# Kernel tuning notes

Hardware: AMD Instinct MI355X
Metric: run time of the kernel (lower is better)

## Reference

```python
import jax, jax.numpy as jnp
import numpy as np

B, C, N, T = 8, 32, 4000, 12
KT = 3
TS = 6          # tem_size
SUP_ORD_CH = (2 * 3 + 1) * C  # (order*support_len+1)*c_in = 224
EPS = 1e-5


def setup_inputs() -> dict:
    key = jax.random.key(0)
    ks = jax.random.split(key, 20)
    inp = {
        "x": jax.random.normal(ks[0], (B, C, N, T), dtype=jnp.float32),
        # dense normalized supports (scaled uniform, like row-normalized adjacency)
        "A0": jax.random.uniform(ks[1], (N, N), dtype=jnp.float32) / N,
        "A1": jax.random.uniform(ks[2], (N, N), dtype=jnp.float32) / N,
        "A2": jax.random.uniform(ks[3], (N, N), dtype=jnp.float32) / N,
        # conv1: 1x1 Conv2d(32 -> 32), bias
        "conv1_w": jax.random.normal(ks[4], (C, C), dtype=jnp.float32) * 0.05,
        "conv1_b": jnp.zeros((C,), dtype=jnp.float32),
        # multigcn mlp: Conv2d(224 -> 64, kernel (1, Kt)), bias
        "mlp_w": jax.random.normal(ks[5], (2 * C, SUP_ORD_CH, 1, KT), dtype=jnp.float32) * 0.02,
        "mlp_b": jnp.zeros((2 * C,), dtype=jnp.float32),
        # conv_temp1: 1x1 Conv2d over time axis (10 -> 6), bias
        "ct1_w": jax.random.normal(ks[6], (TS, T - KT + 1), dtype=jnp.float32) * 0.1,
        "ct1_b": jnp.zeros((TS,), dtype=jnp.float32),
        # TATT_1 params
        "tat_c1_w": jax.random.normal(ks[7], (C,), dtype=jnp.float32) * 0.1,   # Conv2d(c_in->1,1x1,no bias)
        "tat_c2_w": jax.random.normal(ks[8], (N,), dtype=jnp.float32) * 0.01,  # Conv2d(N->1,1x1,no bias)
        "tat_w": jax.random.normal(ks[9], (N, C), dtype=jnp.float32) * 0.01,
        "tat_bias": jnp.zeros((TS, TS), dtype=jnp.float32),
        "tat_v": jax.random.normal(ks[10], (TS, TS), dtype=jnp.float32) * 0.3,
        "bn1_g": jnp.ones((TS,), dtype=jnp.float32),
        "bn1_b": jnp.zeros((TS,), dtype=jnp.float32),
        # final BatchNorm2d(c_out)
        "bn2_g": jnp.ones((C,), dtype=jnp.float32),
        "bn2_b": jnp.zeros((C,), dtype=jnp.float32),
    }
    return inp


def reference(x, A0, A1, A2, conv1_w, conv1_b, mlp_w, mlp_b, ct1_w, ct1_b,
              tat_c1_w, tat_c2_w, tat_w, tat_bias, tat_v, bn1_g, bn1_b,
              bn2_g, bn2_b):
    # residual = conv1(x)  (1x1 conv over channels)
    residual = jnp.einsum('oc,bcnl->bonl', conv1_w, x) + conv1_b[None, :, None, None]

    # multi_gcn_time: nconv does A<-A.T then einsum('ncvl,vw->ncwl'),
    # i.e. out[..,w,..] = sum_v x[..,v,..] * A[w,v]
    outs = [x]
    for A in (A0, A1, A2):
        x1 = jnp.einsum('bcvl,wv->bcwl', x, A)
        outs.append(x1)
        x2 = jnp.einsum('bcvl,wv->bcwl', x1, A)
        outs.append(x2)
    h = jnp.concatenate(outs, axis=1)  # (B, 224, N, T)
    h = jax.lax.conv_general_dilated(
        h, mlp_w, window_strides=(1, 1), padding='VALID',
        dimension_numbers=('NCHW', 'OIHW', 'NCHW')) + mlp_b[None, :, None, None]  # (B,64,N,10)

    # gated tanh * sigmoid
    x1, x2 = jnp.split(h, 2, axis=1)
    g = jnp.tanh(x1) * jax.nn.sigmoid(x2)  # (B,32,N,10)

    # conv_temp1: 1x1 conv over the TIME axis (10 -> 6)
    g = jnp.einsum('ql,bcnl->bcnq', ct1_w, g) + ct1_b[None, None, None, :]  # (B,32,N,6)

    # TATT_1 temporal attention coefficients
    f1 = jnp.einsum('c,bcnt->btn', tat_c1_w, g)                       # (B,6,N)
    f2 = jnp.einsum('n,bcnt->bct', tat_c2_w, g)                       # (B,32,6)
    logits = jax.nn.sigmoid(jnp.einsum('btn,nc,bcs->bts', f1, tat_w, f2) + tat_bias)
    logits = jnp.einsum('ts,bsq->btq', tat_v, logits)                 # (B,6,6)
    # BatchNorm1d(tem_size) applied after permute(0,2,1): channel = q axis
    lp = jnp.transpose(logits, (0, 2, 1))
    mu = lp.mean(axis=(0, 2), keepdims=True)
    var = lp.var(axis=(0, 2), keepdims=True)
    lp = (lp - mu) / jnp.sqrt(var + EPS) * bn1_g[None, :, None] + bn1_b[None, :, None]
    logits = jnp.transpose(lp, (0, 2, 1))
    coefs = jax.nn.softmax(logits, axis=-1)                           # (B,6,6)

    # x = einsum('bcnl,blq->bcnq', x, T_coef.transpose(-1,-2))
    Tc = jnp.transpose(coefs, (0, 2, 1))
    out = jnp.einsum('bcnl,blq->bcnq', g, Tc)                         # (B,32,N,6)

    y = out + residual[:, :, :, -out.shape[3]:]
    # BatchNorm2d(c_out), training-mode batch stats
    mu2 = y.mean(axis=(0, 2, 3), keepdims=True)
    var2 = y.var(axis=(0, 2, 3), keepdims=True)
    return (y - mu2) / jnp.sqrt(var2 + EPS) * bn2_g[None, :, None, None] + bn2_b[None, :, None, None]
```

## Files before the change

### kernel.cpp

```cpp
#include <hip/hip_runtime.h>
#include <hip/hip_bf16.h>
#include <cstdint>
#include <cstddef>


typedef __attribute__((ext_vector_type(8))) short s16x8;
typedef __attribute__((ext_vector_type(4))) short s16x4;
typedef __attribute__((ext_vector_type(4))) float f32x4;

#define DEVFN __device__ __forceinline__

DEVFN void gload16(const void* g, void* l) {
  __builtin_amdgcn_global_load_lds((const __attribute__((address_space(1))) unsigned int*)g,
                                   (__attribute__((address_space(3))) unsigned int*)l, 16, 0, 0);
}

DEVFN unsigned short f2bf(float f) {
  union { float f; unsigned int u; } v; v.f = f;
  unsigned int u = v.u;
  return (unsigned short)((u + 0x7fffu + ((u >> 16) & 1u)) >> 16);
}

__global__ void k_transpose(const float* __restrict__ x,
                            unsigned short* __restrict__ Xt,
                            unsigned short* __restrict__ Scat) {
  __shared__ float ldsT[32 * 417];
  int v0 = blockIdx.x * 32;
  int b = blockIdx.y;
  int tid = threadIdx.x;
  for (int i = tid; i < 1024; i += 256) {
    int c = i >> 5, vv = i & 31;
    const float* src = x + ((size_t)(b * 32 + c) * 4000 + v0 + vv) * 12;
    f32x4 a0 = *(const f32x4*)(src);
    f32x4 a1 = *(const f32x4*)(src + 4);
    f32x4 a2 = *(const f32x4*)(src + 8);
    float* d = ldsT + c * 417 + vv * 13;
    d[0] = a0.x; d[1] = a0.y; d[2] = a0.z; d[3] = a0.w;
    d[4] = a1.x; d[5] = a1.y; d[6] = a1.z; d[7] = a1.w;
    d[8] = a2.x; d[9] = a2.y; d[10] = a2.z; d[11] = a2.w;
  }
  __syncthreads();
  for (int unit = tid; unit < 384; unit += 256) {
    int l = unit >> 5, c = unit & 31;
    alignas(16) unsigned short tmp[32];
#pragma unroll
    for (int vv = 0; vv < 32; ++vv) tmp[vv] = f2bf(ldsT[c * 417 + vv * 13 + l]);
    unsigned short* dst = Xt + (size_t)(b * 384 + l * 32 + c) * 4096 + v0;
#pragma unroll
    for (int j = 0; j < 4; ++j) *(s16x8*)(dst + j * 8) = *(const s16x8*)(tmp + j * 8);
  }
  for (int unit = tid; unit < 384; unit += 256) {
    int l = unit >> 5, vv = unit & 31;
    alignas(16) unsigned short tmp[32];
#pragma unroll
    for (int c = 0; c < 32; ++c) tmp[c] = f2bf(ldsT[c * 417 + vv * 13 + l]);
    unsigned short* dst = Scat + ((size_t)(b * 4000 + v0 + vv) * 12 + l) * 224;
#pragma unroll
    for (int j = 0; j < 4; ++j) *(s16x8*)(dst + j * 8) = *(const s16x8*)(tmp + j * 8);
  }
}

__global__ void k_castA(const float* __restrict__ A, unsigned short* __restrict__ Abf) {
  int idx = blockIdx.x * 256 + threadIdx.x;
  int r = idx >> 10;
  int c4 = (idx & 1023) << 2;
  alignas(8) unsigned short o[4] = {0, 0, 0, 0};
  if (r < 4000 && c4 < 4000) {
    f32x4 v = *(const f32x4*)(A + (size_t)r * 4000 + c4);
    o[0] = f2bf(v.x); o[1] = f2bf(v.y); o[2] = f2bf(v.z); o[3] = f2bf(v.w);
  }
  *(s16x4*)(Abf + (size_t)r * 4096 + c4) = *(const s16x4*)o;
}

__global__ void k_wcat(const float* __restrict__ mlp_w, unsigned short* __restrict__ Wcat) {
  int i = blockIdx.x * 256 + threadIdx.x;
  if (i >= 64 * 672) return;
  int oc = i / 672, k = i % 672;
  int kt = k / 224, ic = k % 224;
  Wcat[i] = f2bf(mlp_w[((size_t)oc * 224 + ic) * 3 + kt]);
}

#define MFMA_(a, b, c) __builtin_amdgcn_mfma_f32_16x16x32_bf16(a, b, c, 0, 0, 0)

#define STGA(d, t) do {                                                          \
    const unsigned short* _s = aSrc + (size_t)(t) * 64;                          \
    unsigned short* _l = smem + (d) * 12288;                                     \
    gload16(_s,          _l + tid * 8);                                          \
    gload16(_s + 262144, _l + (512 + tid) * 8);                                  \
    gload16(_s + 524288, _l + (1024 + tid) * 8);                                 \
  } while (0)

#define STGB(d, h, t) do {                                                       \
    const unsigned short* _s = bSrc + (size_t)(h) * 524288 + (size_t)(t) * 64;   \
    unsigned short* _l = smem + 24576 + ((d) * 2 + (h)) * 8192;                  \
    gload16(_s,          _l + tid * 8);                                          \
    gload16(_s + 262144, _l + (512 + tid) * 8);                                  \
  } while (0)

#define LDA_(d, f, kk) (*(const s16x8*)(smem + (d) * 12288 + aoff + (f) * 1024 + ((kk) ? sxor : 0)))
#define LDB_(d, nf, kk) (*(const s16x8*)(smem + 24576 + ((d) * 2 + hb) * 8192 + boff + (nf) * 1024 + ((kk) ? sxor : 0)))

#define PHASE(d, mp, FIRST, STAGE_CODE, VM) do {                                 \
    s16x8 a00 = LDA_(d, 2 * (mp), 0),     a01 = LDA_(d, 2 * (mp), 1);            \
    s16x8 a10 = LDA_(d, 2 * (mp) + 1, 0), a11 = LDA_(d, 2 * (mp) + 1, 1);        \
    if (FIRST) {                                                                 \
      _Pragma("unroll")                                                          \
      for (int nf = 0; nf < 4; ++nf) { bfr[nf][0] = LDB_(d, nf, 0); bfr[nf][1] = LDB_(d, nf, 1); } \
    }                                                                            \
    STAGE_CODE;                                                                  \
    if (VM) asm volatile("s_waitcnt vmcnt(2)" ::: "memory");                     \
    __builtin_amdgcn_s_barrier();                                                \
    asm volatile("s_waitcnt lgkmcnt(0)" ::: "memory");                           \
    __builtin_amdgcn_s_setprio(1);                                               \
    _Pragma("unroll")                                                            \
    for (int nf = 0; nf < 4; ++nf) {                                             \
      acc[2 * (mp)][nf]     = MFMA_(a00, bfr[nf][0], acc[2 * (mp)][nf]);         \
      acc[2 * (mp)][nf]     = MFMA_(a01, bfr[nf][1], acc[2 * (mp)][nf]);         \
      acc[2 * (mp) + 1][nf] = MFMA_(a10, bfr[nf][0], acc[2 * (mp) + 1][nf]);     \
      acc[2 * (mp) + 1][nf] = MFMA_(a11, bfr[nf][1], acc[2 * (mp) + 1][nf]);     \
    }                                                                            \
    __builtin_amdgcn_s_setprio(0);                                               \
  } while (0)

template <int WRITE_C1>
__global__ __launch_bounds__(512, 2)
void k_gemm(const unsigned short* __restrict__ P, const unsigned short* __restrict__ Q,
            unsigned short* __restrict__ C1, unsigned short* __restrict__ Scat, int jcol) {
  extern __shared__ unsigned short smem[];
  int tid = threadIdx.x;
  int w = tid >> 6, lane = tid & 63;
  int lr = lane & 15, g = lane >> 4;
  int mq = w >> 2, nq = w & 3;
  int bid = blockIdx.x;
  int xcd = bid & 7, lid = bid >> 3;
  int nt = xcd * 2 + (lid >> 4);
  int mt = lid & 15;
  int m0 = mt * 192, n0 = nt * 256;
  int hb = nq >> 1;
  int slot0 = (g ^ (lr & 7)) * 8;
  int sxor = (slot0 & 32) ? -32 : 32;
  int aoff = (mq * 96 + lr) * 64 + slot0;
  int boff = ((nq & 1) * 64 + lr) * 64 + slot0;
  int gk = ((tid & 7) ^ ((tid >> 3) & 7)) * 8;
  const unsigned short* aSrc = P + (size_t)(m0 + (tid >> 3)) * 4096 + gk;
  const unsigned short* bSrc = Q + (size_t)(n0 + (tid >> 3)) * 4096 + gk;
  f32x4 acc[6][4] = {};
  s16x8 bfr[4][2];

  STGA(0, 0);
  STGB(0, 0, 0); STGB(0, 1, 0);
  STGB(1, 0, 1);
  asm volatile("s_waitcnt vmcnt(2)" ::: "memory");
  __builtin_amdgcn_s_barrier();

#pragma unroll 1
  for (int i = 0; i < 32; ++i) {
    int t1 = 2 * i + 1, t2 = 2 * i + 2, t3 = 2 * i + 3;
    PHASE(0, 0, 1, STGB(1, 1, t1), 0);
    PHASE(0, 1, 0, STGA(1, t1),    0);
    PHASE(0, 2, 0, STGB(0, 0, t2), 1);
    PHASE(1, 0, 1, STGB(0, 1, t2), 0);
    PHASE(1, 1, 0, STGA(0, t2),    0);
    PHASE(1, 2, 0, STGB(1, 0, t3), 1);
  }

  asm volatile("s_waitcnt vmcnt(0) lgkmcnt(0)" ::: "memory");
  __syncthreads();
  unsigned short* eld = smem;
  int rb = g * 4;
#pragma unroll
  for (int f = 0; f < 6; ++f)
#pragma unroll
    for (int nf = 0; nf < 4; ++nf)
#pragma unroll
      for (int r = 0; r < 4; ++r)
        eld[(mq * 96 + f * 16 + rb + r) * 264 + nq * 64 + nf * 16 + lr] = f2bf(acc[f][nf][r]);
  __syncthreads();
  if (WRITE_C1) {
#pragma unroll
    for (int uu = 0; uu < 2; ++uu) {
      int u = uu * 512 + tid;
      if (u < 768) {
        int row = u >> 2, q = u & 3;
        unsigned short* dst = C1 + (size_t)(m0 + row) * 4096 + n0 + q * 64;
        const unsigned short* sp = eld + row * 264 + q * 64;
#pragma unroll
        for (int j = 0; j < 8; ++j) *(s16x8*)(dst + j * 8) = *(const s16x8*)(sp + j * 8);
      }
    }
  }
  int bb2 = m0 / 384, lb = (m0 % 384) >> 5;
#pragma unroll
  for (int uu = 0; uu < 3; ++uu) {
    int u = uu * 512 + tid;
    int lg = u >> 8, nl = u & 255;
    int node = n0 + nl;
    if (node < 4000) {
      alignas(16) unsigned short tmp[32];
#pragma unroll
      for (int c = 0; c < 32; ++c) tmp[c] = eld[(lg * 32 + c) * 264 + nl];
      unsigned short* d2 = Scat + ((size_t)(bb2 * 4000 + node) * 12 + lb + lg) * 224 + jcol;
#pragma unroll
      for (int j = 0; j < 4; ++j) *(s16x8*)(d2 + j * 8) = *(const s16x8*)(tmp + j * 8);
    }
  }
}

#define MLPSTG(L, BUF) do {                                                   \
    _Pragma("unroll")                                                         \
    for (int j = 0; j < 7; ++j) {                                             \
      int u = j * 256 + tid;                                                  \
      int s = u >> 6, bn = u & 63;                                            \
      gload16(Scat + ((size_t)(bn0 + bn) * 12 + (L)) * 224 + s * 8,           \
              lds + (BUF) * 14336 + u * 8);                                   \
    }                                                                         \
  } while (0)

__global__ __launch_bounds__(256, 2)
void k_mlp(const unsigned short* __restrict__ Wcat, const unsigned short* __restrict__ Scat,
           const float* __restrict__ mlp_b, float* __restrict__ G) {
  __shared__ unsigned short lds[2 * 14336];
  int tid = threadIdx.x;
  int bn0 = blockIdx.x * 64;
  int w = tid >> 6, lane = tid & 63;
  int lr = lane & 15, g = lane >> 4;
  int p = w & 1, q = w >> 1;
  const unsigned short* w1 = Wcat + (size_t)(p * 16 + lr) * 672 + g * 8;
  const unsigned short* w2 = w1 + 32 * 672;
  f32x4 acc[3][4];

  MLPSTG(0, 0);
  asm volatile("s_waitcnt vmcnt(0)" ::: "memory");
  __syncthreads();

#pragma unroll
  for (int l = 0; l < 12; ++l) {
    if (l < 11) MLPSTG(l + 1, (l + 1) & 1);
    if (l <= 9) {
#pragma unroll
      for (int f = 0; f < 4; ++f) acc[l % 3][f] = (f32x4){0.f, 0.f, 0.f, 0.f};
    }
    const unsigned short* sb = lds + (l & 1) * 14336;
#pragma unroll
    for (int kt = 0; kt < 3; ++kt) {
      int t = l - kt;
      if (t < 0 || t > 9) continue;
      int st = t % 3;
#pragma unroll
      for (int ks = 0; ks < 7; ++ks) {
        s16x8 a1 = *(const s16x8*)(w1 + kt * 224 + ks * 32);
        s16x8 a2 = *(const s16x8*)(w2 + kt * 224 + ks * 32);
        const unsigned short* bbase = sb + ((ks * 4 + g) * 64 + q * 32 + lr) * 8;
        s16x8 b0 = *(const s16x8*)(bbase);
        s16x8 b1 = *(const s16x8*)(bbase + 128);
        acc[st][0] = MFMA_(a1, b0, acc[st][0]);
        acc[st][1] = MFMA_(a1, b1, acc[st][1]);
        acc[st][2] = MFMA_(a2, b0, acc[st][2]);
        acc[st][3] = MFMA_(a2, b1, acc[st][3]);
      }
    }
    if (l >= 2) {
      int t = l - 2, st = t % 3;
#pragma unroll
      for (int bf = 0; bf < 2; ++bf) {
        int nglob = bn0 + q * 32 + bf * 16 + lr;
        int b = nglob / 4000, nn = nglob - b * 4000;
        float* gout = G + ((size_t)(b * 10 + t) * 32) * 4096 + nn;
#pragma unroll
        for (int r = 0; r < 4; ++r) {
          int c = p * 16 + g * 4 + r;
          float v1 = acc[st][bf][r] + mlp_b[c];
          float v2 = acc[st][2 + bf][r] + mlp_b[c + 32];
          gout[(size_t)c * 4096] = tanhf(v1) * (1.0f / (1.0f + __expf(-v2)));
        }
      }
    }
    asm volatile("s_waitcnt vmcnt(0)" ::: "memory");
    __syncthreads();
  }
}

__global__ void k_ct1(const float* __restrict__ G, const float* __restrict__ ct1_w,
                      const float* __restrict__ ct1_b, float* __restrict__ g6) {
  int idx = blockIdx.x * 256 + threadIdx.x;
  if (idx >= 8 * 32 * 4000) return;
  int n = idx % 4000;
  int c = (idx / 4000) % 32;
  int b = idx / (4000 * 32);
  const float* gp = G + ((size_t)(b * 10) * 32 + c) * 4096 + n;
  float v[10];
#pragma unroll
  for (int l = 0; l < 10; ++l) v[l] = gp[(size_t)l * 32 * 4096];
  float* o = g6 + (size_t)idx * 6;
#pragma unroll
  for (int q = 0; q < 6; ++q) {
    float a = ct1_b[q];
#pragma unroll
    for (int l = 0; l < 10; ++l) a += ct1_w[q * 10 + l] * v[l];
    o[q] = a;
  }
}

__global__ void k_f1(const float* __restrict__ g6, const float* __restrict__ c1,
                     float* __restrict__ f1) {
  int idx = blockIdx.x * 128 + threadIdx.x;
  if (idx >= 8 * 4000) return;
  int n = idx % 4000, b = idx / 4000;
  float acc[6] = {};
  const float* gp = g6 + ((size_t)b * 32 * 4000 + n) * 6;
  for (int c = 0; c < 32; ++c) {
    float wv = c1[c];
    const float* p = gp + (size_t)c * 4000 * 6;
#pragma unroll
    for (int t = 0; t < 6; ++t) acc[t] += wv * p[t];
  }
  for (int t = 0; t < 6; ++t) f1[((size_t)b * 6 + t) * 4000 + n] = acc[t];
}

__global__ void k_f2(const float* __restrict__ g6, const float* __restrict__ c2,
                     float* __restrict__ f2) {
  __shared__ float red[256 * 6];
  int bc = blockIdx.x;
  int tid = threadIdx.x;
  float acc[6] = {};
  const float* gp = g6 + (size_t)bc * 4000 * 6;
  for (int n = tid; n < 4000; n += 256) {
    float wv = c2[n];
#pragma unroll
    for (int t = 0; t < 6; ++t) acc[t] += wv * gp[(size_t)n * 6 + t];
  }
  for (int t = 0; t < 6; ++t) red[tid * 6 + t] = acc[t];
  __syncthreads();
  for (int s = 128; s > 0; s >>= 1) {
    if (tid < s)
      for (int t = 0; t < 6; ++t) red[tid * 6 + t] += red[(tid + s) * 6 + t];
    __syncthreads();
  }
  if (tid < 6) f2[bc * 6 + tid] = red[tid];
}

__global__ void k_m1(const float* __restrict__ f1, const float* __restrict__ tw,
                     float* __restrict__ m1) {
  __shared__ float red[8][32];
  int bt = blockIdx.x;
  int nc = blockIdx.y;
  int tid = threadIdx.x;
  int c = tid & 31, gi = tid >> 5;
  float acc = 0.f;
  const float* fp = f1 + (size_t)bt * 4000 + nc * 250;
  const float* twp = tw + ((size_t)nc * 250) * 32 + c;
  for (int n = gi; n < 250; n += 8) acc += fp[n] * twp[n * 32];
  red[gi][c] = acc;
  __syncthreads();
  if (tid < 32) {
    float s = 0.f;
#pragma unroll
    for (int gg = 0; gg < 8; ++gg) s += red[gg][c];
    atomicAdd(&m1[(size_t)bt * 32 + c], s);
  }
}

__global__ void k_att(const float* __restrict__ m1, const float* __restrict__ f2,
                      const float* __restrict__ bias, const float* __restrict__ tv,
                      const float* __restrict__ g1, const float* __restrict__ b1,
                      float* __restrict__ coefs) {
  __shared__ float sig[48 * 6], lgs[48 * 6], mu[6], iv[6];
  int tid = threadIdx.x;
  int b = tid / 6, t = tid % 6;
  if (tid < 48) {
    for (int s = 0; s < 6; ++s) {
      float a = bias[t * 6 + s];
      for (int c = 0; c < 32; ++c)
        a += m1[((size_t)b * 6 + t) * 32 + c] * f2[((size_t)b * 32 + c) * 6 + s];
      sig[tid * 6 + s] = 1.0f / (1.0f + __expf(-a));
    }
  }
  __syncthreads();
  if (tid < 48) {
    for (int q = 0; q < 6; ++q) {
      float a = 0.f;
      for (int s = 0; s < 6; ++s) a += tv[t * 6 + s] * sig[(b * 6 + s) * 6 + q];
      lgs[tid * 6 + q] = a;
    }
  }
  __syncthreads();
  if (tid < 6) {
    float s = 0, s2 = 0;
    for (int r = 0; r < 48; ++r) { float v = lgs[r * 6 + tid]; s += v; s2 += v * v; }
    float m = s / 48.f;
    mu[tid] = m;
    iv[tid] = rsqrtf(s2 / 48.f - m * m + 1e-5f);
  }
  __syncthreads();
  if (tid < 48) {
    float v[6], mx = -1e30f;
    for (int q = 0; q < 6; ++q) {
      v[q] = (lgs[tid * 6 + q] - mu[q]) * iv[q] * g1[q] + b1[q];
      mx = fmaxf(mx, v[q]);
    }
    float s = 0;
    for (int q = 0; q < 6; ++q) { v[q] = __expf(v[q] - mx); s += v[q]; }
    float inv = 1.0f / s;
    for (int q = 0; q < 6; ++q) coefs[tid * 6 + q] = v[q] * inv;
  }
}

__global__ void k_final1(const float* __restrict__ x, const float* __restrict__ cw,
                         const float* __restrict__ cb, const float* __restrict__ g6,
                         const float* __restrict__ coefs, float* __restrict__ out) {
  __shared__ float xt[32 * 8 * 6];
  __shared__ float cwT[1024];
  __shared__ float cfs[36], cbs[32];
  int n0 = blockIdx.x * 8;
  int b = blockIdx.y;
  int tid = threadIdx.x;
  {
    int ci = tid >> 3, seg = tid & 7;
    const float* xp = x + ((size_t)(b * 32 + ci) * 4000 + n0 + seg) * 12 + 6;
#pragma unroll
    for (int q = 0; q < 6; ++q) xt[(ci * 8 + seg) * 6 + q] = xp[q];
  }
  for (int i = tid; i < 1024; i += 256) { int o = i >> 5, ci = i & 31; cwT[ci * 32 + o] = cw[i]; }
  if (tid < 36) cfs[tid] = coefs[b * 36 + tid];
  if (tid < 32) cbs[tid] = cb[tid];
  __syncthreads();
  int nn = tid & 7, c = tid >> 3;
  const float* gp = g6 + ((size_t)(b * 32 + c) * 4000 + n0 + nn) * 6;
  float gv[6];
#pragma unroll
  for (int l = 0; l < 6; ++l) gv[l] = gp[l];
  float y[6];
#pragma unroll
  for (int q = 0; q < 6; ++q) {
    float at = 0.f;
#pragma unroll
    for (int l = 0; l < 6; ++l) at += gv[l] * cfs[q * 6 + l];
    y[q] = at + cbs[c];
  }
  for (int ci = 0; ci < 32; ++ci) {
    float wv = cwT[ci * 32 + c];
#pragma unroll
    for (int q = 0; q < 6; ++q) y[q] += wv * xt[(ci * 8 + nn) * 6 + q];
  }
  float* op = out + ((size_t)(b * 32 + c) * 4000 + n0 + nn) * 6;
#pragma unroll
  for (int q = 0; q < 6; ++q) op[q] = y[q];
}

__global__ void k_stats(const float* __restrict__ out, float* __restrict__ stats) {
  __shared__ float r1[4], r2[4];
  int bc = blockIdx.y;
  int c = bc & 31;
  int tid = threadIdx.x;
  const float* p = out + (size_t)bc * 24000 + blockIdx.x * 6000;
  float s = 0.f, s2 = 0.f;
  for (int i = tid * 4; i < 6000; i += 1024) {
    f32x4 v = *(const f32x4*)(p + i);
    s  += v.x + v.y + v.z + v.w;
    s2 += v.x * v.x + v.y * v.y + v.z * v.z + v.w * v.w;
  }
#pragma unroll
  for (int off = 32; off > 0; off >>= 1) {
    s  += __shfl_down(s, off);
    s2 += __shfl_down(s2, off);
  }
  int lane = tid & 63, w = tid >> 6;
  if (lane == 0) { r1[w] = s; r2[w] = s2; }
  __syncthreads();
  if (tid == 0) {
    atomicAdd(&stats[c],      r1[0] + r1[1] + r1[2] + r1[3]);
    atomicAdd(&stats[32 + c], r2[0] + r2[1] + r2[2] + r2[3]);
  }
}

__global__ void k_final2(float* __restrict__ out, const float* __restrict__ stats,
                         const float* __restrict__ g2, const float* __restrict__ b2) {
  int idx = (blockIdx.x * 256 + threadIdx.x) * 4;
  if (idx >= 6144000) return;
  int c = (idx / 24000) % 32;
  float mean = stats[c] * (1.0f / 192000.f);
  float var = stats[32 + c] * (1.0f / 192000.f) - mean * mean;
  float sc = rsqrtf(var + 1e-5f) * g2[c];
  float sh = b2[c] - mean * sc;
  f32x4 v = *(f32x4*)(out + idx);
  v.x = v.x * sc + sh; v.y = v.y * sc + sh; v.z = v.z * sc + sh; v.w = v.w * sc + sh;
  *(f32x4*)(out + idx) = v;
}

extern "C" void kernel_launch(void* const* d_in, const int* in_sizes, int n_in,
                              void* d_out, int out_size, void* d_ws, size_t ws_size,
                              hipStream_t stream) {
  (void)in_sizes; (void)n_in; (void)out_size;
  const float* x       = (const float*)d_in[0];
  const float* A[3]    = {(const float*)d_in[1], (const float*)d_in[2], (const float*)d_in[3]};
  const float* conv1_w = (const float*)d_in[4];
  const float* conv1_b = (const float*)d_in[5];
  const float* mlp_w   = (const float*)d_in[6];
  const float* mlp_b   = (const float*)d_in[7];
  const float* ct1_w   = (const float*)d_in[8];
  const float* ct1_b   = (const float*)d_in[9];
  const float* c1w     = (const float*)d_in[10];
  const float* c2w     = (const float*)d_in[11];
  const float* tw      = (const float*)d_in[12];
  const float* tbias   = (const float*)d_in[13];
  const float* tv      = (const float*)d_in[14];
  const float* bn1g    = (const float*)d_in[15];
  const float* bn1b    = (const float*)d_in[16];
  const float* bn2g    = (const float*)d_in[17];
  const float* bn2b    = (const float*)d_in[18];
  float* out = (float*)d_out;

  char* ws = (char*)d_ws;
  size_t off = 0;
  auto alloc = [&](size_t bytes) { size_t r = off; off += (bytes + 255) & ~(size_t)255; return r; };
  size_t oScat = alloc(172032000);
  size_t oXt   = alloc(25165824);
  size_t oA    = alloc(33554432);
  size_t oY1t  = alloc(25165824);
  size_t oWcat = alloc(86016);
  size_t oF1 = alloc(768000);
  size_t oF2 = alloc(6144);
  size_t oM1 = alloc(6144);
  size_t oCf = alloc(1152);
  size_t oSt = alloc(256);
  if (ws_size < off) return;

  unsigned short* Scat = (unsigned short*)(ws + oScat);
  unsigned short* Xt   = (unsigned short*)(ws + oXt);
  float*          g6   = (float*)(ws + oXt);
  unsigned short* Abf  = (unsigned short*)(ws + oA);
  float*          G    = (float*)(ws + oA);
  unsigned short* Y1t  = (unsigned short*)(ws + oY1t);
  unsigned short* Wcat = (unsigned short*)(ws + oWcat);

  hipFuncSetAttribute((const void*)k_gemm<0>, hipFuncAttributeMaxDynamicSharedMemorySize, 114688);
  hipFuncSetAttribute((const void*)k_gemm<1>, hipFuncAttributeMaxDynamicSharedMemorySize, 114688);

  hipMemsetAsync(Xt, 0, 25165824, stream);
  hipMemsetAsync(ws + oSt, 0, 256, stream);
  hipMemsetAsync(ws + oM1, 0, 6144, stream);
  k_transpose<<<dim3(125, 8), 256, 0, stream>>>(x, Xt, Scat);
  k_wcat<<<168, 256, 0, stream>>>(mlp_w, Wcat);
  for (int i = 0; i < 3; ++i) {
    k_castA<<<16384, 256, 0, stream>>>(A[i], Abf);
    k_gemm<1><<<256, 512, 114688, stream>>>(Xt, Abf, Y1t, Scat, (2 * i + 1) * 32);
    k_gemm<0><<<256, 512, 114688, stream>>>(Y1t, Abf, nullptr, Scat, (2 * i + 2) * 32);
  }
  k_mlp<<<500, 256, 0, stream>>>(Wcat, Scat, mlp_b, G);
  k_ct1<<<4000, 256, 0, stream>>>(G, ct1_w, ct1_b, g6);
  k_f1<<<250, 128, 0, stream>>>(g6, c1w, (float*)(ws + oF1));
  k_f2<<<256, 256, 0, stream>>>(g6, c2w, (float*)(ws + oF2));
  k_m1<<<dim3(48, 16), 256, 0, stream>>>((float*)(ws + oF1), tw, (float*)(ws + oM1));
  k_att<<<1, 64, 0, stream>>>((float*)(ws + oM1), (float*)(ws + oF2), tbias, tv, bn1g, bn1b,
                              (float*)(ws + oCf));
  k_final1<<<dim3(500, 8), 256, 0, stream>>>(x, conv1_w, conv1_b, g6, (float*)(ws + oCf), out);
  k_stats<<<dim3(4, 256), 256, 0, stream>>>(out, (float*)(ws + oSt));
  k_final2<<<6000, 256, 0, stream>>>(out, (float*)(ws + oSt), bn2g, bn2b);
}
```

Before: 808.6 us.

## Fuse conv_temp1 into gated MLP kernel and retile Scat for contiguous staging

Changes the Scat concat buffer to a tiled layout (time step, 64-node group, 28 slots of 8 channels, node), so each MLP block stages one contiguous chunk per time step. The MLP kernel moves to 512 threads with weights held in registers, and it accumulates the conv_temp1 time projection directly into per-thread sums. That removes the full G intermediate write and the separate k_ct1 kernel. In exchange, register pressure rises (42 weight vectors per thread), and the GEMM epilogue stores to Scat become strided.

```diff
diff --git a/kernel.cpp b/kernel.cpp
--- a/kernel.cpp
+++ b/kernel.cpp
@@ -54,9 +54,10 @@
     alignas(16) unsigned short tmp[32];
 #pragma unroll
     for (int c = 0; c < 32; ++c) tmp[c] = f2bf(ldsT[c * 417 + vv * 13 + l]);
-    unsigned short* dst = Scat + ((size_t)(b * 4000 + v0 + vv) * 12 + l) * 224;
-#pragma unroll
-    for (int j = 0; j < 4; ++j) *(s16x8*)(dst + j * 8) = *(const s16x8*)(tmp + j * 8);
+    int bn = b * 4000 + v0 + vv;
+    unsigned short* dst = Scat + ((((size_t)l * 500 + (bn >> 6)) * 28) * 64 + (bn & 63)) * 8;
+#pragma unroll
+    for (int j = 0; j < 4; ++j) *(s16x8*)(dst + j * 512) = *(const s16x8*)(tmp + j * 8);
   }
 }
 
@@ -74,9 +75,15 @@
 
 __global__ void k_wcat(const float* __restrict__ mlp_w, unsigned short* __restrict__ Wcat) {
   int i = blockIdx.x * 256 + threadIdx.x;
-  if (i >= 64 * 672) return;
-  int oc = i / 672, k = i % 672;
-  int kt = k / 224, ic = k % 224;
+  if (i >= 43008) return;
+  int e = i & 7;
+  int j = (i >> 3) % 21;
+  int rs = (i >> 3) / 21;
+  int s = rs & 1, row = rs >> 1;
+  int kt = j / 7, ks = j % 7;
+  int p2 = row >> 6, g = (row >> 4) & 3, lr = row & 15;
+  int oc = (s ? 32 : 0) + p2 * 16 + lr;
+  int ic = ks * 32 + g * 8 + e;
   Wcat[i] = f2bf(mlp_w[((size_t)oc * 224 + ic) * 3 + kt]);
 }
 
@@ -125,7 +132,7 @@
 template <int WRITE_C1>
 __global__ __launch_bounds__(512, 2)
 void k_gemm(const unsigned short* __restrict__ P, const unsigned short* __restrict__ Q,
-            unsigned short* __restrict__ C1, unsigned short* __restrict__ Scat, int jcol) {
+            unsigned short* __restrict__ C1, unsigned short* __restrict__ Scat, int jslot) {
   extern __shared__ unsigned short smem[];
   int tid = threadIdx.x;
   int w = tid >> 6, lane = tid & 63;
@@ -199,35 +206,49 @@
       alignas(16) unsigned short tmp[32];
 #pragma unroll
       for (int c = 0; c < 32; ++c) tmp[c] = eld[(lg * 32 + c) * 264 + nl];
-      unsigned short* d2 = Scat + ((size_t)(bb2 * 4000 + node) * 12 + lb + lg) * 224 + jcol;
-#pragma unroll
-      for (int j = 0; j < 4; ++j) *(s16x8*)(d2 + j * 8) = *(const s16x8*)(tmp + j * 8);
-    }
-  }
-}
-
-#define MLPSTG(L, BUF) do {                                                   \
-    _Pragma("unroll")                                                         \
-    for (int j = 0; j < 7; ++j) {                                             \
-      int u = j * 256 + tid;                                                  \
-      int s = u >> 6, bn = u & 63;                                            \
-      gload16(Scat + ((size_t)(bn0 + bn) * 12 + (L)) * 224 + s * 8,           \
-              lds + (BUF) * 14336 + u * 8);                                   \
-    }                                                                         \
+      int bn = bb2 * 4000 + node;
+      int l2 = lb + lg;
+      unsigned short* d2 = Scat + ((((size_t)l2 * 500 + (bn >> 6)) * 28 + jslot) * 64 + (bn & 63)) * 8;
+#pragma unroll
+      for (int j = 0; j < 4; ++j) *(s16x8*)(d2 + j * 512) = *(const s16x8*)(tmp + j * 8);
+    }
+  }
+}
+
+#define MLPSTG(L, BUF) do {                                                    \
+    const unsigned short* _sb = Scat + ((size_t)(L) * 500 + grp) * 14336;      \
+    unsigned short* _lb = lds + (BUF) * 14336;                                 \
+    gload16(_sb + tid * 8,          _lb + tid * 8);                            \
+    gload16(_sb + (512 + tid) * 8,  _lb + (512 + tid) * 8);                    \
+    gload16(_sb + (1024 + tid) * 8, _lb + (1024 + tid) * 8);                   \
+    if (tid < 256) gload16(_sb + (1536 + tid) * 8, _lb + (1536 + tid) * 8);    \
   } while (0)
 
-__global__ __launch_bounds__(256, 2)
+__global__ __launch_bounds__(512, 2)
 void k_mlp(const unsigned short* __restrict__ Wcat, const unsigned short* __restrict__ Scat,
-           const float* __restrict__ mlp_b, float* __restrict__ G) {
+           const float* __restrict__ mlp_b, const float* __restrict__ ct1_w,
+           const float* __restrict__ ct1_b, float* __restrict__ g6) {
   __shared__ unsigned short lds[2 * 14336];
   int tid = threadIdx.x;
-  int bn0 = blockIdx.x * 64;
+  int grp = blockIdx.x;
   int w = tid >> 6, lane = tid & 63;
   int lr = lane & 15, g = lane >> 4;
-  int p = w & 1, q = w >> 1;
-  const unsigned short* w1 = Wcat + (size_t)(p * 16 + lr) * 672 + g * 8;
-  const unsigned short* w2 = w1 + 32 * 672;
-  f32x4 acc[3][4];
+  int p2 = w & 1, bnq = w >> 1;
+  const unsigned short* wrow = Wcat + (size_t)(((p2 * 4 + g) * 16 + lr) * 2) * 168;
+  s16x8 wa[21], wb[21];
+#pragma unroll
+  for (int j = 0; j < 21; ++j) {
+    wa[j] = *(const s16x8*)(wrow + j * 8);
+    wb[j] = *(const s16x8*)(wrow + 168 + j * 8);
+  }
+  float mb1[4], mb2[4];
+#pragma unroll
+  for (int r = 0; r < 4; ++r) {
+    mb1[r] = mlp_b[p2 * 16 + g * 4 + r];
+    mb2[r] = mlp_b[32 + p2 * 16 + g * 4 + r];
+  }
+  f32x4 acc[3][2];
+  float g6a[4][6] = {};
 
   MLPSTG(0, 0);
   asm volatile("s_waitcnt vmcnt(0)" ::: "memory");
@@ -237,8 +258,8 @@
   for (int l = 0; l < 12; ++l) {
     if (l < 11) MLPSTG(l + 1, (l + 1) & 1);
     if (l <= 9) {
-#pragma unroll
-      for (int f = 0; f < 4; ++f) acc[l % 3][f] = (f32x4){0.f, 0.f, 0.f, 0.f};
+      acc[l % 3][0] = (f32x4){0.f, 0.f, 0.f, 0.f};
+      acc[l % 3][1] = (f32x4){0.f, 0.f, 0.f, 0.f};
     }
     const unsigned short* sb = lds + (l & 1) * 14336;
 #pragma unroll
@@ -248,56 +269,35 @@
       int st = t % 3;
 #pragma unroll
       for (int ks = 0; ks < 7; ++ks) {
-        s16x8 a1 = *(const s16x8*)(w1 + kt * 224 + ks * 32);
-        s16x8 a2 = *(const s16x8*)(w2 + kt * 224 + ks * 32);
-        const unsigned short* bbase = sb + ((ks * 4 + g) * 64 + q * 32 + lr) * 8;
-        s16x8 b0 = *(const s16x8*)(bbase);
-        s16x8 b1 = *(const s16x8*)(bbase + 128);
-        acc[st][0] = MFMA_(a1, b0, acc[st][0]);
-        acc[st][1] = MFMA_(a1, b1, acc[st][1]);
-        acc[st][2] = MFMA_(a2, b0, acc[st][2]);
-        acc[st][3] = MFMA_(a2, b1, acc[st][3]);
+        int j = kt * 7 + ks;
+        s16x8 bb = *(const s16x8*)(sb + ((ks * 4 + g) * 64 + bnq * 16 + lr) * 8);
+        acc[st][0] = MFMA_(wa[j], bb, acc[st][0]);
+        acc[st][1] = MFMA_(wb[j], bb, acc[st][1]);
       }
     }
     if (l >= 2) {
       int t = l - 2, st = t % 3;
 #pragma unroll
-      for (int bf = 0; bf < 2; ++bf) {
-        int nglob = bn0 + q * 32 + bf * 16 + lr;
-        int b = nglob / 4000, nn = nglob - b * 4000;
-        float* gout = G + ((size_t)(b * 10 + t) * 32) * 4096 + nn;
-#pragma unroll
-        for (int r = 0; r < 4; ++r) {
-          int c = p * 16 + g * 4 + r;
-          float v1 = acc[st][bf][r] + mlp_b[c];
-          float v2 = acc[st][2 + bf][r] + mlp_b[c + 32];
-          gout[(size_t)c * 4096] = tanhf(v1) * (1.0f / (1.0f + __expf(-v2)));
-        }
+      for (int r = 0; r < 4; ++r) {
+        float v1 = acc[st][0][r] + mb1[r];
+        float v2 = acc[st][1][r] + mb2[r];
+        float gg = tanhf(v1) * (1.0f / (1.0f + __expf(-v2)));
+#pragma unroll
+        for (int q6 = 0; q6 < 6; ++q6) g6a[r][q6] += ct1_w[q6 * 10 + t] * gg;
       }
     }
     asm volatile("s_waitcnt vmcnt(0)" ::: "memory");
     __syncthreads();
   }
-}
-
-__global__ void k_ct1(const float* __restrict__ G, const float* __restrict__ ct1_w,
-                      const float* __restrict__ ct1_b, float* __restrict__ g6) {
-  int idx = blockIdx.x * 256 + threadIdx.x;
-  if (idx >= 8 * 32 * 4000) return;
-  int n = idx % 4000;
-  int c = (idx / 4000) % 32;
-  int b = idx / (4000 * 32);
-  const float* gp = G + ((size_t)(b * 10) * 32 + c) * 4096 + n;
-  float v[10];
-#pragma unroll
-  for (int l = 0; l < 10; ++l) v[l] = gp[(size_t)l * 32 * 4096];
-  float* o = g6 + (size_t)idx * 6;
-#pragma unroll
-  for (int q = 0; q < 6; ++q) {
-    float a = ct1_b[q];
-#pragma unroll
-    for (int l = 0; l < 10; ++l) a += ct1_w[q * 10 + l] * v[l];
-    o[q] = a;
+
+  int nglob = grp * 64 + bnq * 16 + lr;
+  int b = nglob / 4000, nn = nglob - b * 4000;
+#pragma unroll
+  for (int r = 0; r < 4; ++r) {
+    int c = p2 * 16 + g * 4 + r;
+    float* op = g6 + ((size_t)(b * 32 + c) * 4000 + nn) * 6;
+#pragma unroll
+    for (int q6 = 0; q6 < 6; ++q6) op[q6] = g6a[r][q6] + ct1_b[q6];
   }
 }
 
@@ -529,7 +529,6 @@
   unsigned short* Xt   = (unsigned short*)(ws + oXt);
   float*          g6   = (float*)(ws + oXt);
   unsigned short* Abf  = (unsigned short*)(ws + oA);
-  float*          G    = (float*)(ws + oA);
   unsigned short* Y1t  = (unsigned short*)(ws + oY1t);
   unsigned short* Wcat = (unsigned short*)(ws + oWcat);
 
@@ -543,11 +542,10 @@
   k_wcat<<<168, 256, 0, stream>>>(mlp_w, Wcat);
   for (int i = 0; i < 3; ++i) {
     k_castA<<<16384, 256, 0, stream>>>(A[i], Abf);
-    k_gemm<1><<<256, 512, 114688, stream>>>(Xt, Abf, Y1t, Scat, (2 * i + 1) * 32);
-    k_gemm<0><<<256, 512, 114688, stream>>>(Y1t, Abf, nullptr, Scat, (2 * i + 2) * 32);
-  }
-  k_mlp<<<500, 256, 0, stream>>>(Wcat, Scat, mlp_b, G);
-  k_ct1<<<4000, 256, 0, stream>>>(G, ct1_w, ct1_b, g6);
+    k_gemm<1><<<256, 512, 114688, stream>>>(Xt, Abf, Y1t, Scat, (2 * i + 1) * 4);
+    k_gemm<0><<<256, 512, 114688, stream>>>(Y1t, Abf, nullptr, Scat, (2 * i + 2) * 4);
+  }
+  k_mlp<<<500, 512, 0, stream>>>(Wcat, Scat, mlp_b, ct1_w, ct1_b, g6);
   k_f1<<<250, 128, 0, stream>>>(g6, c1w, (float*)(ws + oF1));
   k_f2<<<256, 256, 0, stream>>>(g6, c2w, (float*)(ws + oF2));
   k_m1<<<dim3(48, 16), 256, 0, stream>>>((float*)(ws + oF1), tw, (float*)(ws + oM1));
```

New measurement: 761.2 us. 5.9% less time.
